# Kernel tuning notes

Hardware: AMD Instinct MI355X
Metric: run time of the kernel (lower is better)

The kernel has to match this reference:

```python
import jax, jax.numpy as jnp
import numpy as np

HEADS = 8
DIM_HEAD = 8
UP = 64  # nn.Upsample(scale_factor=64) on the score map
DN = ('NCHW', 'OIHW', 'NCHW')


def setup_inputs() -> dict:
    key = jax.random.key(0)
    ks = jax.random.split(key, 6)
    dim, inner = 64, HEADS * DIM_HEAD
    f = jax.random.normal(ks[0], (1, dim, 64, 64), dtype=jnp.float32)
    w_qkv = jax.random.normal(ks[1], (3 * inner, dim, 1, 1), dtype=jnp.float32) * 0.05
    wq = jax.random.normal(ks[2], (inner, inner, 11, 11), dtype=jnp.float32) * 0.02
    bq = jax.random.normal(ks[3], (inner,), dtype=jnp.float32) * 0.02
    wk = jax.random.normal(ks[4], (inner, inner, 11, 11), dtype=jnp.float32) * 0.02
    bk = jax.random.normal(ks[5], (inner,), dtype=jnp.float32) * 0.02
    return {'f': f, 'w_qkv': w_qkv, 'wq': wq, 'bq': bq, 'wk': wk, 'bk': bk}


def _down_conv(x, w, b):
    # Conv2d(inner, inner, (11,11), stride (8,8), padding 2) + exact GELU
    y = jax.lax.conv_general_dilated(x, w, (8, 8), ((2, 2), (2, 2)), dimension_numbers=DN)
    return jax.nn.gelu(y + b[None, :, None, None], approximate=False)


def _split_heads(t):
    # 'b (h c) x y -> b h c (x y)'
    bb, cc, x, y = t.shape
    return t.reshape(bb, HEADS, cc // HEADS, x * y)


def reference(f, w_qkv, wq, bq, wk, bk):
    b, _, H, W = f.shape
    scale = DIM_HEAD ** -0.5
    # 1x1 conv qkv projection, no bias
    qkv = jax.lax.conv_general_dilated(f, w_qkv, (1, 1), ((0, 0), (0, 0)), dimension_numbers=DN)
    q, k, v = jnp.split(qkv, 3, axis=1)
    q = _split_heads(_down_conv(q, wq, bq)) * scale  # [b,h,c,n_low]
    k = _split_heads(_down_conv(k, wk, bk))          # [b,h,c,n_low]
    v = _split_heads(v)                              # [b,h,c,HW]
    dots = jnp.einsum('bhci,bhcj->bhij', q, k)       # [b,h,n_low,n_low]
    # nearest-neighbor upsample by 64 on both score dims -> [b,h,HW,HW]
    dots = jnp.repeat(jnp.repeat(dots, UP, axis=2), UP, axis=3)
    attn = jax.nn.softmax(dots, axis=-1)
    fmap = jnp.einsum('bhij,bhcj->bhci', attn, v)    # [b,h,c,HW]
    return fmap.reshape(b, HEADS * DIM_HEAD, H, W)
```

## Files before the change

kernel.cpp:

```cpp
#include <hip/hip_runtime.h>

#define SCALE 0.35355339059327379f
#define RSQRT2 0.70710678118654752f

#define PL      4624
#define QP_OFF  0
#define KP_OFF  (64*PL)
#define VP_OFF  (2*64*PL)
#define QA_OFF  (VP_OFF + 4*4096)
#define KA_OFF  (QA_OFF + 4096)

__global__ __launch_bounds__(384) void k1(const float* __restrict__ f,
                                          const float* __restrict__ w_qkv,
                                          float* __restrict__ ws)
{
    __shared__ float sm[14656];
    const int b = blockIdx.x, t = threadIdx.x;
    const int x = b >> 1, yh = b & 1;
    float* wt = sm;
    float* fl = sm + 12352;

    if (t < 64) (ws + QA_OFF)[b*64 + t] = 0.f;

    {
        float* plane = ws + (yh ? KP_OFF : QP_OFF) + x*PL;
        for (int j = t; j < 528; j += 384) {
            int idx;
            if (j < 272) {
                const int rp = j / 68, c = j % 68;
                const int row = (rp < 2) ? rp : rp + 64;
                idx = row*68 + c;
            } else {
                const int jj = j - 272;
                const int cp = jj >> 6, r2 = (jj & 63) + 2;
                const int col = (cp < 2) ? cp : cp + 64;
                idx = r2*68 + col;
            }
            plane[idx] = 0.f;
        }
    }
    #pragma unroll
    for (int j = 0; j < 8; ++j) {
        const int idx = t + 384*j;
        const float4 v = *(const float4*)(w_qkv + 4*idx);
        const int oc = idx >> 4, ic0 = (4*idx) & 63;
        wt[(ic0+0)*193 + oc] = v.x;
        wt[(ic0+1)*193 + oc] = v.y;
        wt[(ic0+2)*193 + oc] = v.z;
        wt[(ic0+3)*193 + oc] = v.w;
    }
    for (int i = t; i < 512; i += 384) {
        const int ic = i >> 3, p = i & 7;
        *(float4*)&fl[ic*36 + p*4] = *(const float4*)(f + ic*4096 + x*64 + yh*32 + p*4);
    }
    __syncthreads();

    const int w = t >> 6, lane = t & 63;
    const int type = w >> 1, yoct = w & 1;
    float acc[16];
    #pragma unroll
    for (int j = 0; j < 16; ++j) acc[j] = 0.f;
    #pragma unroll 4
    for (int ic = 0; ic < 64; ++ic) {
        const float wv = wt[ic*193 + type*64 + lane];
        const float4 p0 = *(const float4*)&fl[ic*36 + yoct*16];
        const float4 p1 = *(const float4*)&fl[ic*36 + yoct*16 + 4];
        const float4 p2 = *(const float4*)&fl[ic*36 + yoct*16 + 8];
        const float4 p3 = *(const float4*)&fl[ic*36 + yoct*16 + 12];
        acc[0]  = fmaf(wv, p0.x, acc[0]);  acc[1]  = fmaf(wv, p0.y, acc[1]);
        acc[2]  = fmaf(wv, p0.z, acc[2]);  acc[3]  = fmaf(wv, p0.w, acc[3]);
        acc[4]  = fmaf(wv, p1.x, acc[4]);  acc[5]  = fmaf(wv, p1.y, acc[5]);
        acc[6]  = fmaf(wv, p1.z, acc[6]);  acc[7]  = fmaf(wv, p1.w, acc[7]);
        acc[8]  = fmaf(wv, p2.x, acc[8]);  acc[9]  = fmaf(wv, p2.y, acc[9]);
        acc[10] = fmaf(wv, p2.z, acc[10]); acc[11] = fmaf(wv, p2.w, acc[11]);
        acc[12] = fmaf(wv, p3.x, acc[12]); acc[13] = fmaf(wv, p3.y, acc[13]);
        acc[14] = fmaf(wv, p3.z, acc[14]); acc[15] = fmaf(wv, p3.w, acc[15]);
    }
    if (type < 2) {
        float* plane = ws + (type ? KP_OFF : QP_OFF) + lane*PL;
        const int base = (x + 2)*68 + yh*32 + yoct*16 + 2;
        #pragma unroll
        for (int j = 0; j < 8; ++j)
            *(float2*)(plane + base + 2*j) = make_float2(acc[2*j], acc[2*j+1]);
    } else {
        float s = 0.f;
        #pragma unroll
        for (int j = 0; j < 16; ++j) s += acc[j];
        (ws + VP_OFF)[(yh*2 + yoct)*4096 + x*64 + lane] = s * 0.015625f;
    }
}

__global__ __launch_bounds__(512) void k2(const float* __restrict__ ws_qP,
                                          const float* __restrict__ ws_kP,
                                          const float* __restrict__ wq,
                                          const float* __restrict__ wk,
                                          float* __restrict__ qa,
                                          float* __restrict__ ka)
{
    const int b = blockIdx.x, t = threadIdx.x;
    const int type = b >> 7, ic = (b >> 1) & 63, khh = b & 1;
    const int kh0 = khh ? 6 : 0, nkh = khh ? 5 : 6;
    const float* plane = (type ? ws_kP : ws_qP) + ic*PL;
    const float* wsrc  = (type ? wk : wq) + ic*121 + kh0*11;
    const int lane = t & 63;
    const int oc0 = __builtin_amdgcn_readfirstlane(t >> 6) * 8;
    const int ox = lane >> 3, oy = lane & 7;

    float acc[8] = {0.f,0.f,0.f,0.f,0.f,0.f,0.f,0.f};
    #pragma unroll
    for (int khl = 0; khl < 6; ++khl) {
        if (khl < nkh) {
            const int xp = ox*8 + kh0 + khl;
            const float* prow = plane + xp*68 + oy*8;
            const float4 r0 = *(const float4*)(prow);
            const float4 r1 = *(const float4*)(prow + 4);
            const float4 r2 = *(const float4*)(prow + 8);
            const float pr[12] = {r0.x,r0.y,r0.z,r0.w, r1.x,r1.y,r1.z,r1.w,
                                  r2.x,r2.y,r2.z,r2.w};
            const float* wrow = wsrc + khl*11;
            #pragma unroll
            for (int kw = 0; kw < 11; ++kw) {
                const float pv = pr[kw];
                #pragma unroll
                for (int j = 0; j < 8; ++j) {
                    const float wgt = wrow[(oc0 + j)*7744 + kw];
                    acc[j] = fmaf(wgt, pv, acc[j]);
                }
            }
        }
    }
    float* ab = (type ? ka : qa) + lane;
    #pragma unroll
    for (int j = 0; j < 8; ++j)
        atomicAdd(ab + (oc0 + j)*64, acc[j]);
}

__global__ __launch_bounds__(512) void k3(const float* __restrict__ qa,
                                          const float* __restrict__ ka,
                                          const float* __restrict__ Vpart,
                                          const float* __restrict__ bq,
                                          const float* __restrict__ bk,
                                          float* __restrict__ out)
{
    __shared__ float vrow[64*65];
    __shared__ float kg[4096];
    const int x = blockIdx.x, t = threadIdx.x;
    for (int idx = t; idx < 4096; idx += 512) {
        const int jl = idx >> 6, ch = idx & 63;
        float s = 0.f;
        #pragma unroll
        for (int p = 0; p < 4; ++p) s += Vpart[p*4096 + jl*64 + ch];
        vrow[ch*65 + jl] = s;
        const int oc = jl, il = ch;
        const float v = ka[oc*64 + il] + bk[oc];
        kg[oc*64 + il] = 0.5f*v*(1.0f + erff(v*RSQRT2));
    }
    __syncthreads();
    const int h = t >> 6, lane = t & 63;
    float qg[8];
    #pragma unroll
    for (int c = 0; c < 8; ++c) {
        const int oc = h*8 + c;
        const float v = qa[oc*64 + x] + bq[oc];
        qg[c] = 0.5f*v*(1.0f + erff(v*RSQRT2));
    }
    float d = 0.f;
    #pragma unroll
    for (int c = 0; c < 8; ++c)
        d = fmaf(qg[c], kg[(h*8 + c)*64 + lane], d);
    d *= SCALE;
    float m = d;
    #pragma unroll
    for (int mm = 1; mm < 64; mm <<= 1) m = fmaxf(m, __shfl_xor(m, mm, 64));
    const float e = __expf(d - m);
    float ssum = e;
    #pragma unroll
    for (int mm = 1; mm < 64; mm <<= 1) ssum += __shfl_xor(ssum, mm, 64);
    const float p = e / ssum;
    #pragma unroll
    for (int c = 0; c < 8; ++c) {
        float r = p * vrow[(h*8 + c)*65 + lane];
        #pragma unroll
        for (int mm = 1; mm < 64; mm <<= 1) r += __shfl_xor(r, mm, 64);
        out[(h*8 + c)*4096 + x*64 + lane] = r;
    }
}

extern "C" void kernel_launch(void* const* d_in, const int* in_sizes, int n_in,
                              void* d_out, int out_size, void* d_ws, size_t ws_size,
                              hipStream_t stream) {
    const float* f     = (const float*)d_in[0];
    const float* w_qkv = (const float*)d_in[1];
    const float* wq    = (const float*)d_in[2];
    const float* bq    = (const float*)d_in[3];
    const float* wk    = (const float*)d_in[4];
    const float* bk    = (const float*)d_in[5];
    float* out = (float*)d_out;
    float* ws  = (float*)d_ws;

    k1<<<128, 384, 0, stream>>>(f, w_qkv, ws);
    k2<<<256, 512, 0, stream>>>(ws + QP_OFF, ws + KP_OFF, wq, wk,
                                ws + QA_OFF, ws + KA_OFF);
    k3<<<64, 512, 0, stream>>>(ws + QA_OFF, ws + KA_OFF, ws + VP_OFF,
                               bq, bk, out);
}
```

Baseline: 30.78 us.

## Repack conv weights in k1 and restructure down-conv to avoid atomics

k1 gets extra blocks that copy the 11x11 conv weights for q and k into a padded layout (rows of 12 floats) in the workspace, so k2 can read them with aligned float4 loads. k2 is reorganized so each block owns four output channels at one output row and reduces over input channels in shared memory. This removes the float atomicAdds and the zeroing of the accumulators, and bias plus GELU are applied in k2 instead of k3. The cost is repacking the weights on every call and writing and then rereading that padded copy through global memory.

```diff
diff --git a/kernel.cpp b/kernel.cpp
--- a/kernel.cpp
+++ b/kernel.cpp
@@ -7,20 +7,46 @@
 #define QP_OFF  0
 #define KP_OFF  (64*PL)
 #define VP_OFF  (2*64*PL)
-#define QA_OFF  (VP_OFF + 4*4096)
-#define KA_OFF  (QA_OFF + 4096)
+#define WP_OFF  (VP_OFF + 4*4096)
+#define WP_SZ   (2*64*64*132)
+#define QD_OFF  (WP_OFF + WP_SZ)
+#define KD_OFF  (QD_OFF + 4096)
 
 __global__ __launch_bounds__(384) void k1(const float* __restrict__ f,
                                           const float* __restrict__ w_qkv,
+                                          const float* __restrict__ wq,
+                                          const float* __restrict__ wk,
                                           float* __restrict__ ws)
 {
     __shared__ float sm[14656];
     const int b = blockIdx.x, t = threadIdx.x;
+
+    if (b >= 128) {
+        const int rb = b - 128;
+        const int type = rb >> 6, oc = rb & 63;
+        const float* wsrc = (type ? wk : wq) + oc*7744;
+        float* wdst = ws + WP_OFF + (size_t)(type*64 + oc)*64*132;
+        float* wl = sm;
+        #pragma unroll
+        for (int j = 0; j < 6; ++j) {
+            const int idx = t + 384*j;
+            if (idx < 1936)
+                *(float4*)&wl[4*idx] = *(const float4*)(wsrc + 4*idx);
+        }
+        __syncthreads();
+        for (int p = t; p < 704; p += 384) {
+            const int ic = p / 11, kh = p % 11;
+            const float* s = &wl[ic*121 + kh*11];
+            float* d = &wdst[ic*132 + kh*12];
+            #pragma unroll
+            for (int kw = 0; kw < 11; ++kw) d[kw] = s[kw];
+        }
+        return;
+    }
+
     const int x = b >> 1, yh = b & 1;
     float* wt = sm;
     float* fl = sm + 12352;
-
-    if (t < 64) (ws + QA_OFF)[b*64 + t] = 0.f;
 
     {
         float* plane = ws + (yh ? KP_OFF : QP_OFF) + x*PL;
@@ -92,58 +118,60 @@
 
 __global__ __launch_bounds__(512) void k2(const float* __restrict__ ws_qP,
                                           const float* __restrict__ ws_kP,
-                                          const float* __restrict__ wq,
-                                          const float* __restrict__ wk,
-                                          float* __restrict__ qa,
-                                          float* __restrict__ ka)
-{
-    const int b = blockIdx.x, t = threadIdx.x;
-    const int type = b >> 7, ic = (b >> 1) & 63, khh = b & 1;
-    const int kh0 = khh ? 6 : 0, nkh = khh ? 5 : 6;
-    const float* plane = (type ? ws_kP : ws_qP) + ic*PL;
-    const float* wsrc  = (type ? wk : wq) + ic*121 + kh0*11;
-    const int lane = t & 63;
-    const int oc0 = __builtin_amdgcn_readfirstlane(t >> 6) * 8;
-    const int ox = lane >> 3, oy = lane & 7;
-
-    float acc[8] = {0.f,0.f,0.f,0.f,0.f,0.f,0.f,0.f};
-    #pragma unroll
-    for (int khl = 0; khl < 6; ++khl) {
-        if (khl < nkh) {
-            const int xp = ox*8 + kh0 + khl;
-            const float* prow = plane + xp*68 + oy*8;
-            const float4 r0 = *(const float4*)(prow);
-            const float4 r1 = *(const float4*)(prow + 4);
-            const float4 r2 = *(const float4*)(prow + 8);
-            const float pr[12] = {r0.x,r0.y,r0.z,r0.w, r1.x,r1.y,r1.z,r1.w,
-                                  r2.x,r2.y,r2.z,r2.w};
-            const float* wrow = wsrc + khl*11;
-            #pragma unroll
-            for (int kw = 0; kw < 11; ++kw) {
-                const float pv = pr[kw];
-                #pragma unroll
-                for (int j = 0; j < 8; ++j) {
-                    const float wgt = wrow[(oc0 + j)*7744 + kw];
-                    acc[j] = fmaf(wgt, pv, acc[j]);
-                }
-            }
-        }
-    }
-    float* ab = (type ? ka : qa) + lane;
-    #pragma unroll
-    for (int j = 0; j < 8; ++j)
-        atomicAdd(ab + (oc0 + j)*64, acc[j]);
-}
-
-__global__ __launch_bounds__(512) void k3(const float* __restrict__ qa,
-                                          const float* __restrict__ ka,
-                                          const float* __restrict__ Vpart,
+                                          const float* __restrict__ wPad,
                                           const float* __restrict__ bq,
                                           const float* __restrict__ bk,
+                                          float* __restrict__ qd,
+                                          float* __restrict__ kd)
+{
+    __shared__ float red[512];
+    const int b = blockIdx.x, t = threadIdx.x;
+    const int type = b >> 7, ox = (b >> 4) & 7, ocg = b & 15;
+    const float* planes = type ? ws_kP : ws_qP;
+    const int oc2 = t >> 7, ick = (t >> 3) & 15, oy = t & 7;
+    const int oc = ocg*4 + oc2;
+    const float* wbase = wPad + (size_t)(type*64 + oc)*64*132;
+
+    float a0 = 0.f, a1 = 0.f;
+    for (int j = 0; j < 4; ++j) {
+        const int ic = ick + 16*j;
+        const float* pl = planes + ic*PL + (ox*8)*68 + oy*8;
+        const float* wr = wbase + ic*132;
+        #pragma unroll
+        for (int kh = 0; kh < 11; ++kh) {
+            const float4 r0 = *(const float4*)(pl + kh*68);
+            const float4 r1 = *(const float4*)(pl + kh*68 + 4);
+            const float4 r2 = *(const float4*)(pl + kh*68 + 8);
+            const float4 w0 = *(const float4*)(wr + kh*12);
+            const float4 w1 = *(const float4*)(wr + kh*12 + 4);
+            const float4 w2 = *(const float4*)(wr + kh*12 + 8);
+            a0 = fmaf(w0.x, r0.x, a0); a1 = fmaf(w0.y, r0.y, a1);
+            a0 = fmaf(w0.z, r0.z, a0); a1 = fmaf(w0.w, r0.w, a1);
+            a0 = fmaf(w1.x, r1.x, a0); a1 = fmaf(w1.y, r1.y, a1);
+            a0 = fmaf(w1.z, r1.z, a0); a1 = fmaf(w1.w, r1.w, a1);
+            a0 = fmaf(w2.x, r2.x, a0); a1 = fmaf(w2.y, r2.y, a1);
+            a0 = fmaf(w2.z, r2.z, a0);
+        }
+    }
+    red[t] = a0 + a1;
+    __syncthreads();
+    if (t < 32) {
+        const int ro = t >> 3, ry = t & 7;
+        float s = 0.f;
+        #pragma unroll
+        for (int k = 0; k < 16; ++k) s += red[ro*128 + k*8 + ry];
+        const int occ = ocg*4 + ro;
+        const float v = s + (type ? bk[occ] : bq[occ]);
+        (type ? kd : qd)[occ*64 + ox*8 + ry] = 0.5f*v*(1.0f + erff(v*RSQRT2));
+    }
+}
+
+__global__ __launch_bounds__(512) void k3(const float* __restrict__ qd,
+                                          const float* __restrict__ kd,
+                                          const float* __restrict__ Vpart,
                                           float* __restrict__ out)
 {
     __shared__ float vrow[64*65];
-    __shared__ float kg[4096];
     const int x = blockIdx.x, t = threadIdx.x;
     for (int idx = t; idx < 4096; idx += 512) {
         const int jl = idx >> 6, ch = idx & 63;
@@ -151,23 +179,13 @@
         #pragma unroll
         for (int p = 0; p < 4; ++p) s += Vpart[p*4096 + jl*64 + ch];
         vrow[ch*65 + jl] = s;
-        const int oc = jl, il = ch;
-        const float v = ka[oc*64 + il] + bk[oc];
-        kg[oc*64 + il] = 0.5f*v*(1.0f + erff(v*RSQRT2));
     }
     __syncthreads();
     const int h = t >> 6, lane = t & 63;
-    float qg[8];
-    #pragma unroll
-    for (int c = 0; c < 8; ++c) {
-        const int oc = h*8 + c;
-        const float v = qa[oc*64 + x] + bq[oc];
-        qg[c] = 0.5f*v*(1.0f + erff(v*RSQRT2));
-    }
     float d = 0.f;
     #pragma unroll
     for (int c = 0; c < 8; ++c)
-        d = fmaf(qg[c], kg[(h*8 + c)*64 + lane], d);
+        d = fmaf(qd[(h*8 + c)*64 + x], kd[(h*8 + c)*64 + lane], d);
     d *= SCALE;
     float m = d;
     #pragma unroll
@@ -198,9 +216,8 @@
     float* out = (float*)d_out;
     float* ws  = (float*)d_ws;
 
-    k1<<<128, 384, 0, stream>>>(f, w_qkv, ws);
-    k2<<<256, 512, 0, stream>>>(ws + QP_OFF, ws + KP_OFF, wq, wk,
-                                ws + QA_OFF, ws + KA_OFF);
-    k3<<<64, 512, 0, stream>>>(ws + QA_OFF, ws + KA_OFF, ws + VP_OFF,
-                               bq, bk, out);
-}
+    k1<<<256, 384, 0, stream>>>(f, w_qkv, wq, wk, ws);
+    k2<<<256, 512, 0, stream>>>(ws + QP_OFF, ws + KP_OFF, ws + WP_OFF,
+                                bq, bk, ws + QD_OFF, ws + KD_OFF);
+    k3<<<64, 512, 0, stream>>>(ws + QD_OFF, ws + KD_OFF, ws + VP_OFF, out);
+}
```

New measurement: 45.24 us. 1.47x slower.
